# Kernel tuning notes

Measured on AMD Instinct MI355X. Metric: run time of the kernel, lower is better.

The kernel has to match this reference:

```python
import jax, jax.numpy as jnp
import numpy as np

BANDWIDTH = 1.0  # init kwarg: bandwidth; sphere mode -> var_s = gamma = bandwidth
LOG2PI = float(np.log(2.0 * np.pi))


def setup_inputs() -> dict:
    key = jax.random.key(0)
    k1, k2, k3, k4 = jax.random.split(key, 4)
    x = jax.random.normal(k1, (4096, 256), dtype=jnp.float32)
    y = jax.random.normal(k2, (4096, 128), dtype=jnp.float32)
    x_s = jax.random.normal(k3, (8192, 256), dtype=jnp.float32)
    y_s = jax.random.normal(k4, (8192, 128), dtype=jnp.float32)
    return {"x": x, "y": y, "x_s": x_s, "y_s": y_s}


def _sq_dists(a, b):
    # ||a_i - b_j||^2 via GEMM expansion: (batch, num_s)
    a2 = jnp.sum(a * a, axis=-1)[:, None]
    b2 = jnp.sum(b * b, axis=-1)[None, :]
    return a2 + b2 - 2.0 * jnp.einsum("bd,sd->bs", a, b)


def reference(x, y, x_s, y_s):
    x_dim = x.shape[-1]
    y_dim = y.shape[-1]
    var_s = BANDWIDTH
    gamma = BANDWIDTH
    logA_x = x_dim * (LOG2PI + jnp.log(jnp.float32(var_s)))
    logA_y = y_dim * (LOG2PI + jnp.log(jnp.float32(gamma)))

    sdx = _sq_dists(x, x_s) / var_s  # (batch, num_s)
    sdy = _sq_dists(y, y_s) / gamma  # (batch, num_s)

    E_log_pxy = jax.nn.logsumexp(-0.5 * (logA_x + logA_y + sdx + sdy), axis=-1)
    E_log_px = jax.nn.logsumexp(-0.5 * (logA_x + sdx), axis=-1)
    E_log_py = jax.nn.logsumexp(-0.5 * (logA_y + sdy), axis=-1)
    return jnp.mean(E_log_pxy - E_log_px - E_log_py)
```

## Files before the change

### kernel.cpp

```cpp
#include <hip/hip_runtime.h>
#include <hip/hip_bf16.h>
#include <stdint.h>

#define B_N 4096
#define S_N 8192
#define KX  256
#define KY  128
#define BM 128
#define BN 128

typedef __bf16 bf16x8 __attribute__((ext_vector_type(8)));
typedef float  f32x4  __attribute__((ext_vector_type(4)));

#define OFF_XH   ((size_t)0)
#define OFF_YH   ((size_t)2097152)
#define OFF_SXH  ((size_t)3145728)
#define OFF_SYH  ((size_t)7340032)
#define OFF_NX   ((size_t)9437184)
#define OFF_NY   (OFF_NX + 16384)
#define OFF_NSX  (OFF_NY + 16384)
#define OFF_NSY  (OFF_NSX + 32768)
#define OFF_PART (OFF_NSY + 32768)
#define OFF_BSUM (OFF_PART + (size_t)3*64*4096*2*4)

__device__ __forceinline__ void gl2lds16(const void* g, void* l) {
  typedef const __attribute__((address_space(1))) unsigned int* gp_t;
  typedef __attribute__((address_space(3))) unsigned int* lp_t;
  __builtin_amdgcn_global_load_lds((gp_t)g, (lp_t)l, 16, 0, 0);
}

__device__ __forceinline__ unsigned short f2bf(float f) {
  unsigned u = __builtin_bit_cast(unsigned, f);
  return (unsigned short)((u + 0x7fffu + ((u >> 16) & 1u)) >> 16);
}

__global__ __launch_bounds__(256) void conv_all(const float* __restrict__ x,
                                                const float* __restrict__ y,
                                                const float* __restrict__ xs,
                                                const float* __restrict__ ys,
                                                char* __restrict__ ws) {
  int b    = blockIdx.x;
  int wave = threadIdx.x >> 6;
  int lane = threadIdx.x & 63;
  const float* src; unsigned short* hi; float* nrm;
  int K, row;
  if (b < 1024) {
    src = x;  hi = (unsigned short*)(ws + OFF_XH);
    nrm = (float*)(ws + OFF_NX); K = 256; row = b * 4 + wave;
  } else if (b < 2048) {
    src = y;  hi = (unsigned short*)(ws + OFF_YH);
    nrm = (float*)(ws + OFF_NY); K = 128; row = (b - 1024) * 4 + wave;
  } else if (b < 4096) {
    src = xs; hi = (unsigned short*)(ws + OFF_SXH);
    nrm = (float*)(ws + OFF_NSX); K = 256; row = (b - 2048) * 4 + wave;
  } else {
    src = ys; hi = (unsigned short*)(ws + OFF_SYH);
    nrm = (float*)(ws + OFF_NSY); K = 128; row = (b - 4096) * 4 + wave;
  }
  float acc = 0.f;
  if (K == 256) {
    float4 v = ((const float4*)(src + (size_t)row * 256))[lane];
    float vv[4] = {v.x, v.y, v.z, v.w};
    ushort4 h4;
    unsigned short* hp = (unsigned short*)&h4;
    #pragma unroll
    for (int k = 0; k < 4; ++k) {
      hp[k] = f2bf(vv[k]);
      acc = fmaf(vv[k], vv[k], acc);
    }
    ((ushort4*)(hi + (size_t)row * 256))[lane] = h4;
  } else {
    float2 v = ((const float2*)(src + (size_t)row * 128))[lane];
    float vv[2] = {v.x, v.y};
    ushort2 h2;
    unsigned short* hp = (unsigned short*)&h2;
    #pragma unroll
    for (int k = 0; k < 2; ++k) {
      hp[k] = f2bf(vv[k]);
      acc = fmaf(vv[k], vv[k], acc);
    }
    ((ushort2*)(hi + (size_t)row * 128))[lane] = h2;
  }
  #pragma unroll
  for (int o = 32; o > 0; o >>= 1) acc += __shfl_down(acc, o);
  if (lane == 0) nrm[row] = acc;
}

__global__ __launch_bounds__(512, 4) void mie_main(const char* __restrict__ ws,
                                                   float* __restrict__ part) {
  __shared__ __align__(16) char smem[32768];

  const int tid  = threadIdx.x;
  const int lane = tid & 63;
  const int wave = tid >> 6;
  const int c    = lane & 15;
  const int q    = lane >> 4;
  const int wm   = wave >> 1;
  const int wn   = wave & 1;

  const int b     = blockIdx.x;
  const int xcd   = b & 7;
  const int w     = b >> 3;
  const int bm_t  = w & 31;
  const int sn_t  = xcd * 8 + (w >> 5);
  const int bm0   = bm_t * BM;
  const int sn0   = sn_t * BN;

  const char* xh  = ws + OFF_XH;
  const char* yh  = ws + OFF_YH;
  const char* sxh = ws + OFF_SXH;
  const char* syh = ws + OFF_SYH;
  const float* nx  = (const float*)(ws + OFF_NX);
  const float* ny  = (const float*)(ws + OFF_NY);
  const float* nsx = (const float*)(ws + OFF_NSX);
  const float* nsy = (const float*)(ws + OFF_NSY);

  auto stage = [&](int kc, int buf) {
    const char *ah, *bh; int rb, k0b;
    if (kc < 8) { ah = xh; bh = sxh; rb = 512; k0b = kc * 64; }
    else        { ah = yh; bh = syh; rb = 256; k0b = (kc - 8) * 64; }
    char* base = smem + buf * 16384;
    int l  = wave * 64 + lane;
    int r  = l >> 2;
    int sl = l & 3;
    int g  = sl ^ ((r >> 1) & 3);
    size_t kofs = (size_t)k0b + (size_t)g * 16;
    size_t goA  = (size_t)(bm0 + r) * rb + kofs;
    size_t goB  = (size_t)(sn0 + r) * rb + kofs;
    char* dst = base + wave * 1024;
    gl2lds16(ah + goA, dst);
    gl2lds16(bh + goB, dst + 8192);
  };

  const int slot = (q ^ ((c >> 1) & 3)) * 16;
  int aoff[2], boff[4];
  #pragma unroll
  for (int i = 0; i < 2; ++i) aoff[i] = (wm * 32 + i * 16 + c) * 64 + slot;
  #pragma unroll
  for (int j = 0; j < 4; ++j) boff[j] = (wn * 64 + j * 16 + c) * 64 + slot;

  f32x4 accx[2][4], accy[2][4];
  #pragma unroll
  for (int i = 0; i < 2; ++i)
    #pragma unroll
    for (int j = 0; j < 4; ++j) {
      accx[i][j] = (f32x4){0.f,0.f,0.f,0.f};
      accy[i][j] = (f32x4){0.f,0.f,0.f,0.f};
    }

  stage(0, 0);
  __syncthreads();

  for (int kc = 0; kc < 12; ++kc) {
    if (kc < 11) stage(kc + 1, (kc + 1) & 1);
    const char* base = smem + (kc & 1) * 16384;
    bf16x8 Ah[2], Bh[4];
    #pragma unroll
    for (int i = 0; i < 2; ++i) Ah[i] = *(const bf16x8*)(base + aoff[i]);
    #pragma unroll
    for (int j = 0; j < 4; ++j) Bh[j] = *(const bf16x8*)(base + 8192 + boff[j]);
    if (kc < 8) {
      #pragma unroll
      for (int i = 0; i < 2; ++i)
        #pragma unroll
        for (int j = 0; j < 4; ++j)
          accx[i][j] = __builtin_amdgcn_mfma_f32_16x16x32_bf16(Ah[i], Bh[j], accx[i][j], 0, 0, 0);
    } else {
      #pragma unroll
      for (int i = 0; i < 2; ++i)
        #pragma unroll
        for (int j = 0; j < 4; ++j)
          accy[i][j] = __builtin_amdgcn_mfma_f32_16x16x32_bf16(Ah[i], Bh[j], accy[i][j], 0, 0, 0);
    }
    __syncthreads();
  }

  float hxv[2][4], hyv[2][4];
  #pragma unroll
  for (int i = 0; i < 2; ++i)
    #pragma unroll
    for (int r = 0; r < 4; ++r) {
      int rr = bm0 + wm * 32 + i * 16 + q * 4 + r;
      hxv[i][r] = -0.5f * nx[rr];
      hyv[i][r] = -0.5f * ny[rr];
    }
  float hsxv[4], hsyv[4];
  #pragma unroll
  for (int j = 0; j < 4; ++j) {
    int cc = sn0 + wn * 64 + j * 16 + c;
    hsxv[j] = -0.5f * nsx[cc];
    hsyv[j] = -0.5f * nsy[cc];
  }

  float2* xch = (float2*)smem;
  #pragma unroll
  for (int i = 0; i < 2; ++i) {
    #pragma unroll
    for (int r = 0; r < 4; ++r) {
      float vx[4], vy[4];
      #pragma unroll
      for (int j = 0; j < 4; ++j) {
        vx[j] = accx[i][j][r] + hxv[i][r] + hsxv[j];
        vy[j] = accy[i][j][r] + hyv[i][r] + hsyv[j];
      }
      int rl = wm * 32 + i * 16 + q * 4 + r;
      #pragma unroll
      for (int st = 0; st < 3; ++st) {
        float v0 = (st == 0) ? vx[0] + vy[0] : (st == 1 ? vx[0] : vy[0]);
        float v1 = (st == 0) ? vx[1] + vy[1] : (st == 1 ? vx[1] : vy[1]);
        float v2 = (st == 0) ? vx[2] + vy[2] : (st == 1 ? vx[2] : vy[2]);
        float v3 = (st == 0) ? vx[3] + vy[3] : (st == 1 ? vx[3] : vy[3]);
        float m = fmaxf(fmaxf(v0, v1), fmaxf(v2, v3));
        #pragma unroll
        for (int msk = 1; msk < 16; msk <<= 1) m = fmaxf(m, __shfl_xor(m, msk));
        float s = __expf(v0 - m) + __expf(v1 - m) + __expf(v2 - m) + __expf(v3 - m);
        #pragma unroll
        for (int msk = 1; msk < 16; msk <<= 1) s += __shfl_xor(s, msk);
        if (c == 0) xch[(st * 128 + rl) * 2 + wn] = (float2){m, s};
      }
    }
  }
  __syncthreads();

  if (tid < 384) {
    int st = tid >> 7;
    int rl = tid & 127;
    float2 a = xch[(st * 128 + rl) * 2 + 0];
    float2 bb = xch[(st * 128 + rl) * 2 + 1];
    float m = fmaxf(a.x, bb.x);
    float s = a.y * __expf(a.x - m) + bb.y * __expf(bb.x - m);
    size_t idx = ((size_t)st * 64 + sn_t) * B_N + (bm0 + rl);
    ((float2*)part)[idx] = (float2){m, s};
  }
}

__global__ __launch_bounds__(256) void fin1(const float* __restrict__ part,
                                            float* __restrict__ bsum) {
  __shared__ float2 lds[3][4][64];
  int tid  = threadIdx.x;
  int wave = tid >> 6;
  int lane = tid & 63;
  int row  = blockIdx.x * 64 + lane;
  #pragma unroll
  for (int j = 0; j < 3; ++j) {
    float m = -__builtin_inff(), s = 0.f;
    #pragma unroll
    for (int pp = 0; pp < 16; ++pp) {
      int p = wave * 16 + pp;
      float2 a = ((const float2*)part)[((size_t)j * 64 + p) * B_N + row];
      float nm = fmaxf(m, a.x);
      s = s * __expf(m - nm) + a.y * __expf(a.x - nm);
      m = nm;
    }
    lds[j][wave][lane] = (float2){m, s};
  }
  __syncthreads();
  if (wave == 0) {
    float v[3];
    #pragma unroll
    for (int j = 0; j < 3; ++j) {
      float m = -__builtin_inff(), s = 0.f;
      #pragma unroll
      for (int u = 0; u < 4; ++u) {
        float2 a = lds[j][u][lane];
        float nm = fmaxf(m, a.x);
        s = s * __expf(m - nm) + a.y * __expf(a.x - nm);
        m = nm;
      }
      v[j] = m + __logf(s);
    }
    float local = v[0] - v[1] - v[2];
    #pragma unroll
    for (int o = 32; o > 0; o >>= 1) local += __shfl_down(local, o);
    if (lane == 0) bsum[blockIdx.x] = local;
  }
}

__global__ void fin2(const float* __restrict__ bsum, float* __restrict__ out) {
  int t = threadIdx.x;
  float a = bsum[t];
  #pragma unroll
  for (int o = 32; o > 0; o >>= 1) a += __shfl_down(a, o);
  if (t == 0) out[0] = a * (1.0f / (float)B_N);
}

extern "C" void kernel_launch(void* const* d_in, const int* in_sizes, int n_in,
                              void* d_out, int out_size, void* d_ws, size_t ws_size,
                              hipStream_t stream) {
  (void)in_sizes; (void)n_in; (void)out_size; (void)ws_size;
  const float* x  = (const float*)d_in[0];
  const float* y  = (const float*)d_in[1];
  const float* xs = (const float*)d_in[2];
  const float* ys = (const float*)d_in[3];
  char* ws = (char*)d_ws;

  conv_all<<<6144, 256, 0, stream>>>(x, y, xs, ys, ws);
  mie_main<<<2048, 512, 0, stream>>>(ws, (float*)(ws + OFF_PART));
  fin1<<<B_N / 64, 256, 0, stream>>>((const float*)(ws + OFF_PART), (float*)(ws + OFF_BSUM));
  fin2<<<1, 64, 0, stream>>>((const float*)(ws + OFF_BSUM), (float*)d_out);
}
```

Before: 143.9 us.

## Stage two K-chunks per barrier, work in base-2 log domain, widen final reduction

The main kernel now loads two 64-wide K chunks into a 64 KB double buffer per iteration, which halves the number of barriers across the 12 chunks. The inputs are pre-scaled by 1/ln2 and the norms by -0.5/ln2, so the epilogue can use native exp2/log2 instead of expf, with ln2 restored at the end. fin1 now spreads each row's partial merge across 8 lanes and runs 128 blocks instead of 64. The catch is that doubling LDS per block likely lowers occupancy below the 4 blocks the launch bounds ask for, and the bf16 rounding of the scaled values changes slightly.

After: 144.7 us. Within noise of the previous version (+0.5%).

```diff
diff --git a/kernel.cpp b/kernel.cpp
--- a/kernel.cpp
+++ b/kernel.cpp
@@ -6,11 +6,17 @@
 #define S_N 8192
 #define KX  256
 #define KY  128
-#define BM 128
-#define BN 128
+#define BM  128
+#define BN  128
+
+#define INV_LN2 1.4426950408889634f
+#define LN2_F   0.6931471805599453f
 
 typedef __bf16 bf16x8 __attribute__((ext_vector_type(8)));
 typedef float  f32x4  __attribute__((ext_vector_type(4)));
+
+__device__ __forceinline__ float exp2g(float x) { return __builtin_amdgcn_exp2f(x); }
+__device__ __forceinline__ float log2g(float x) { return __builtin_amdgcn_logf(x); }
 
 #define OFF_XH   ((size_t)0)
 #define OFF_YH   ((size_t)2097152)
@@ -43,19 +49,19 @@
   int wave = threadIdx.x >> 6;
   int lane = threadIdx.x & 63;
   const float* src; unsigned short* hi; float* nrm;
-  int K, row;
+  int K, row; float scale;
   if (b < 1024) {
     src = x;  hi = (unsigned short*)(ws + OFF_XH);
-    nrm = (float*)(ws + OFF_NX); K = 256; row = b * 4 + wave;
+    nrm = (float*)(ws + OFF_NX); K = 256; row = b * 4 + wave; scale = INV_LN2;
   } else if (b < 2048) {
     src = y;  hi = (unsigned short*)(ws + OFF_YH);
-    nrm = (float*)(ws + OFF_NY); K = 128; row = (b - 1024) * 4 + wave;
+    nrm = (float*)(ws + OFF_NY); K = 128; row = (b - 1024) * 4 + wave; scale = INV_LN2;
   } else if (b < 4096) {
     src = xs; hi = (unsigned short*)(ws + OFF_SXH);
-    nrm = (float*)(ws + OFF_NSX); K = 256; row = (b - 2048) * 4 + wave;
+    nrm = (float*)(ws + OFF_NSX); K = 256; row = (b - 2048) * 4 + wave; scale = 1.0f;
   } else {
     src = ys; hi = (unsigned short*)(ws + OFF_SYH);
-    nrm = (float*)(ws + OFF_NSY); K = 128; row = (b - 4096) * 4 + wave;
+    nrm = (float*)(ws + OFF_NSY); K = 128; row = (b - 4096) * 4 + wave; scale = 1.0f;
   }
   float acc = 0.f;
   if (K == 256) {
@@ -65,8 +71,8 @@
     unsigned short* hp = (unsigned short*)&h4;
     #pragma unroll
     for (int k = 0; k < 4; ++k) {
-      hp[k] = f2bf(vv[k]);
       acc = fmaf(vv[k], vv[k], acc);
+      hp[k] = f2bf(vv[k] * scale);
     }
     ((ushort4*)(hi + (size_t)row * 256))[lane] = h4;
   } else {
@@ -76,19 +82,19 @@
     unsigned short* hp = (unsigned short*)&h2;
     #pragma unroll
     for (int k = 0; k < 2; ++k) {
-      hp[k] = f2bf(vv[k]);
       acc = fmaf(vv[k], vv[k], acc);
+      hp[k] = f2bf(vv[k] * scale);
     }
     ((ushort2*)(hi + (size_t)row * 128))[lane] = h2;
   }
   #pragma unroll
   for (int o = 32; o > 0; o >>= 1) acc += __shfl_down(acc, o);
-  if (lane == 0) nrm[row] = acc;
+  if (lane == 0) nrm[row] = acc * (-0.5f * INV_LN2);
 }
 
 __global__ __launch_bounds__(512, 4) void mie_main(const char* __restrict__ ws,
                                                    float* __restrict__ part) {
-  __shared__ __align__(16) char smem[32768];
+  __shared__ __align__(16) char smem[65536];
 
   const int tid  = threadIdx.x;
   const int lane = tid & 63;
@@ -115,11 +121,10 @@
   const float* nsx = (const float*)(ws + OFF_NSX);
   const float* nsy = (const float*)(ws + OFF_NSY);
 
-  auto stage = [&](int kc, int buf) {
+  auto stage = [&](int kc, char* base) {
     const char *ah, *bh; int rb, k0b;
     if (kc < 8) { ah = xh; bh = sxh; rb = 512; k0b = kc * 64; }
     else        { ah = yh; bh = syh; rb = 256; k0b = (kc - 8) * 64; }
-    char* base = smem + buf * 16384;
     int l  = wave * 64 + lane;
     int r  = l >> 2;
     int sl = l & 3;
@@ -148,29 +153,40 @@
       accy[i][j] = (f32x4){0.f,0.f,0.f,0.f};
     }
 
-  stage(0, 0);
+  stage(0, smem);
+  stage(1, smem + 16384);
   __syncthreads();
 
-  for (int kc = 0; kc < 12; ++kc) {
-    if (kc < 11) stage(kc + 1, (kc + 1) & 1);
-    const char* base = smem + (kc & 1) * 16384;
-    bf16x8 Ah[2], Bh[4];
-    #pragma unroll
-    for (int i = 0; i < 2; ++i) Ah[i] = *(const bf16x8*)(base + aoff[i]);
-    #pragma unroll
-    for (int j = 0; j < 4; ++j) Bh[j] = *(const bf16x8*)(base + 8192 + boff[j]);
-    if (kc < 8) {
+  #pragma unroll
+  for (int p = 0; p < 6; ++p) {
+    if (p < 5) {
+      char* nb = smem + ((p + 1) & 1) * 32768;
+      stage(2 * p + 2, nb);
+      stage(2 * p + 3, nb + 16384);
+    }
+    const char* bufb = smem + (p & 1) * 32768;
+    #pragma unroll
+    for (int h = 0; h < 2; ++h) {
+      int kc = 2 * p + h;
+      const char* base = bufb + h * 16384;
+      bf16x8 Ah[2], Bh[4];
       #pragma unroll
-      for (int i = 0; i < 2; ++i)
+      for (int i = 0; i < 2; ++i) Ah[i] = *(const bf16x8*)(base + aoff[i]);
+      #pragma unroll
+      for (int j = 0; j < 4; ++j) Bh[j] = *(const bf16x8*)(base + 8192 + boff[j]);
+      if (kc < 8) {
         #pragma unroll
-        for (int j = 0; j < 4; ++j)
-          accx[i][j] = __builtin_amdgcn_mfma_f32_16x16x32_bf16(Ah[i], Bh[j], accx[i][j], 0, 0, 0);
-    } else {
-      #pragma unroll
-      for (int i = 0; i < 2; ++i)
+        for (int i = 0; i < 2; ++i)
+          #pragma unroll
+          for (int j = 0; j < 4; ++j)
+            accx[i][j] = __builtin_amdgcn_mfma_f32_16x16x32_bf16(Ah[i], Bh[j], accx[i][j], 0, 0, 0);
+      } else {
         #pragma unroll
-        for (int j = 0; j < 4; ++j)
-          accy[i][j] = __builtin_amdgcn_mfma_f32_16x16x32_bf16(Ah[i], Bh[j], accy[i][j], 0, 0, 0);
+        for (int i = 0; i < 2; ++i)
+          #pragma unroll
+          for (int j = 0; j < 4; ++j)
+            accy[i][j] = __builtin_amdgcn_mfma_f32_16x16x32_bf16(Ah[i], Bh[j], accy[i][j], 0, 0, 0);
+      }
     }
     __syncthreads();
   }
@@ -181,15 +197,15 @@
     #pragma unroll
     for (int r = 0; r < 4; ++r) {
       int rr = bm0 + wm * 32 + i * 16 + q * 4 + r;
-      hxv[i][r] = -0.5f * nx[rr];
-      hyv[i][r] = -0.5f * ny[rr];
+      hxv[i][r] = nx[rr];
+      hyv[i][r] = ny[rr];
     }
   float hsxv[4], hsyv[4];
   #pragma unroll
   for (int j = 0; j < 4; ++j) {
     int cc = sn0 + wn * 64 + j * 16 + c;
-    hsxv[j] = -0.5f * nsx[cc];
-    hsyv[j] = -0.5f * nsy[cc];
+    hsxv[j] = nsx[cc];
+    hsyv[j] = nsy[cc];
   }
 
   float2* xch = (float2*)smem;
@@ -213,7 +229,7 @@
         float m = fmaxf(fmaxf(v0, v1), fmaxf(v2, v3));
         #pragma unroll
         for (int msk = 1; msk < 16; msk <<= 1) m = fmaxf(m, __shfl_xor(m, msk));
-        float s = __expf(v0 - m) + __expf(v1 - m) + __expf(v2 - m) + __expf(v3 - m);
+        float s = exp2g(v0 - m) + exp2g(v1 - m) + exp2g(v2 - m) + exp2g(v3 - m);
         #pragma unroll
         for (int msk = 1; msk < 16; msk <<= 1) s += __shfl_xor(s, msk);
         if (c == 0) xch[(st * 128 + rl) * 2 + wn] = (float2){m, s};
@@ -228,7 +244,7 @@
     float2 a = xch[(st * 128 + rl) * 2 + 0];
     float2 bb = xch[(st * 128 + rl) * 2 + 1];
     float m = fmaxf(a.x, bb.x);
-    float s = a.y * __expf(a.x - m) + bb.y * __expf(bb.x - m);
+    float s = a.y * exp2g(a.x - m) + bb.y * exp2g(bb.x - m);
     size_t idx = ((size_t)st * 64 + sn_t) * B_N + (bm0 + rl);
     ((float2*)part)[idx] = (float2){m, s};
   }
@@ -236,52 +252,47 @@
 
 __global__ __launch_bounds__(256) void fin1(const float* __restrict__ part,
                                             float* __restrict__ bsum) {
-  __shared__ float2 lds[3][4][64];
-  int tid  = threadIdx.x;
-  int wave = tid >> 6;
-  int lane = tid & 63;
-  int row  = blockIdx.x * 64 + lane;
+  __shared__ float red[4];
+  int tid = threadIdx.x;
+  int sub = tid & 7;
+  int row = blockIdx.x * 32 + (tid >> 3);
+  float v[3];
   #pragma unroll
   for (int j = 0; j < 3; ++j) {
     float m = -__builtin_inff(), s = 0.f;
     #pragma unroll
-    for (int pp = 0; pp < 16; ++pp) {
-      int p = wave * 16 + pp;
+    for (int pp = 0; pp < 8; ++pp) {
+      int p = sub * 8 + pp;
       float2 a = ((const float2*)part)[((size_t)j * 64 + p) * B_N + row];
       float nm = fmaxf(m, a.x);
-      s = s * __expf(m - nm) + a.y * __expf(a.x - nm);
+      s = s * exp2g(m - nm) + a.y * exp2g(a.x - nm);
       m = nm;
     }
-    lds[j][wave][lane] = (float2){m, s};
-  }
+    #pragma unroll
+    for (int msk = 1; msk < 8; msk <<= 1) {
+      float om = __shfl_xor(m, msk);
+      float os = __shfl_xor(s, msk);
+      float nm = fmaxf(m, om);
+      s = s * exp2g(m - nm) + os * exp2g(om - nm);
+      m = nm;
+    }
+    v[j] = m + log2g(s);
+  }
+  float local = (sub == 0) ? (v[0] - v[1] - v[2]) : 0.f;
+  #pragma unroll
+  for (int o = 32; o > 0; o >>= 1) local += __shfl_down(local, o);
+  int wv = tid >> 6, lane = tid & 63;
+  if (lane == 0) red[wv] = local;
   __syncthreads();
-  if (wave == 0) {
-    float v[3];
-    #pragma unroll
-    for (int j = 0; j < 3; ++j) {
-      float m = -__builtin_inff(), s = 0.f;
-      #pragma unroll
-      for (int u = 0; u < 4; ++u) {
-        float2 a = lds[j][u][lane];
-        float nm = fmaxf(m, a.x);
-        s = s * __expf(m - nm) + a.y * __expf(a.x - nm);
-        m = nm;
-      }
-      v[j] = m + __logf(s);
-    }
-    float local = v[0] - v[1] - v[2];
-    #pragma unroll
-    for (int o = 32; o > 0; o >>= 1) local += __shfl_down(local, o);
-    if (lane == 0) bsum[blockIdx.x] = local;
-  }
+  if (tid == 0) bsum[blockIdx.x] = red[0] + red[1] + red[2] + red[3];
 }
 
 __global__ void fin2(const float* __restrict__ bsum, float* __restrict__ out) {
   int t = threadIdx.x;
-  float a = bsum[t];
+  float a = bsum[t] + bsum[t + 64];
   #pragma unroll
   for (int o = 32; o > 0; o >>= 1) a += __shfl_down(a, o);
-  if (t == 0) out[0] = a * (1.0f / (float)B_N);
+  if (t == 0) out[0] = a * (LN2_F / (float)B_N);
 }
 
 extern "C" void kernel_launch(void* const* d_in, const int* in_sizes, int n_in,
@@ -296,6 +307,6 @@
 
   conv_all<<<6144, 256, 0, stream>>>(x, y, xs, ys, ws);
   mie_main<<<2048, 512, 0, stream>>>(ws, (float*)(ws + OFF_PART));
-  fin1<<<B_N / 64, 256, 0, stream>>>((const float*)(ws + OFF_PART), (float*)(ws + OFF_BSUM));
+  fin1<<<128, 256, 0, stream>>>((const float*)(ws + OFF_PART), (float*)(ws + OFF_BSUM));
   fin2<<<1, 64, 0, stream>>>((const float*)(ws + OFF_BSUM), (float*)d_out);
 }
```
